# Kernel optimization log

Hardware: AMD Instinct MI355X
Metric: run time of the kernel (lower is better)

## Reference

```python
import jax, jax.numpy as jnp
import numpy as np

N, A_IN, A_OUT, X_IN, X_OUT, NNODE = 4, 8, 16, 64, 64, 1024


def setup_inputs() -> dict:
    key = jax.random.key(0)
    ks = jax.random.split(key, 32)
    s = 0.02
    inp = {
        'A': jax.random.normal(ks[0], (N, A_IN, NNODE, NNODE), jnp.float32),
        'X': jax.random.normal(ks[1], (N, NNODE, X_IN), jnp.float32),
    }
    # Linear weights stored as (in, out); torch Linear computes x @ W.T with W (out,in)
    for i, k in zip(range(1, 6), ks[2:7]):
        inp[f'A_W{i}'] = jax.random.normal(k, (A_IN, A_OUT), jnp.float32) * s
    inp['A_W6'] = jax.random.normal(ks[7], (X_IN, A_OUT), jnp.float32) * s
    inp['A_W7'] = jax.random.normal(ks[8], (X_IN, A_OUT), jnp.float32) * s
    inp['A_bias'] = jnp.zeros((A_OUT,), jnp.float32)
    for pfx, base in (('X1', 9), ('X2', 16)):
        inp[f'{pfx}_W1'] = jax.random.normal(ks[base], (X_IN, X_OUT), jnp.float32) * s
        inp[f'{pfx}_W2'] = jax.random.normal(ks[base + 1], (X_IN, X_OUT), jnp.float32) * s
        for j in range(3, 7):
            inp[f'{pfx}_W{j}'] = jax.random.normal(ks[base + j - 1], (A_IN, X_OUT), jnp.float32) * s
        inp[f'{pfx}_bias'] = jnp.zeros((X_OUT,), jnp.float32)
    inp['out_W'] = jax.random.normal(ks[23], (A_OUT * X_OUT, X_OUT), jnp.float32) * s
    inp['out_b'] = jnp.zeros((X_OUT,), jnp.float32)
    return inp


def reference(A, X, A_W1, A_W2, A_W3, A_W4, A_W5, A_W6, A_W7, A_bias,
              X1_W1, X1_W2, X1_W3, X1_W4, X1_W5, X1_W6, X1_bias,
              X2_W1, X2_W2, X2_W3, X2_W4, X2_W5, X2_W6, X2_bias,
              out_W, out_b):
    n = A.shape[-1]
    # diag_part: N, n, 1, A_in
    dp = jnp.transpose(jnp.diagonal(A, axis1=-2, axis2=-1), (0, 2, 1))[:, :, None, :]
    mdp = jnp.mean(dp, axis=1, keepdims=True)                 # N,1,1,A_in
    moc = jnp.transpose(jnp.mean(A, axis=-1), (0, 2, 1))[:, :, None, :]  # N,n,1,A_in
    mall = jnp.mean(moc, axis=1, keepdims=True)               # N,1,1,A_in
    mX = jnp.mean(X, axis=-2, keepdims=True)                  # N,1,x_in

    At = jnp.transpose(A, (0, 2, 3, 1)) @ A_W1                # N,n,n,A_out
    At = At + mall @ A_W2
    t3 = moc @ A_W3                                           # N,n,1,A_out (linear commutes with symmetrize)
    At = At + t3 + jnp.swapaxes(t3, 1, 2)
    t6 = X @ A_W6                                             # N,n,A_out
    At = At + t6[:, :, None, :] + t6[:, None, :, :]
    At = At + (mX @ A_W7)[:, None, :, :]
    At = At + A_bias
    At = At + mdp @ A_W4
    t5 = dp @ A_W5
    At = At + t5 + jnp.swapaxes(t5, 1, 2)

    def x_branch(W1, W2, W3, W4, W5, W6, b):
        r = X @ W1 + mX @ W2 + moc[:, :, 0, :] @ W3 + mall[:, 0, :, :] @ W6 + b
        return r + dp[:, :, 0, :] @ W4 + mdp[:, 0, :, :] @ W5  # N,n,x_out

    X1t = x_branch(X1_W1, X1_W2, X1_W3, X1_W4, X1_W5, X1_W6, X1_bias)
    X2t = x_branch(X2_W1, X2_W2, X2_W3, X2_W4, X2_W5, X2_W6, X2_bias)

    out = jnp.einsum('nijs,njt->nist', At, X2t) / n           # N,n,A_out,x_out
    out = out.reshape(out.shape[0], out.shape[1], -1) @ out_W + out_b
    out = out + X1t
    return jnp.transpose(At, (0, 3, 1, 2)), out
```

## Files before the change

### kernel.cpp

```cpp
#include <hip/hip_runtime.h>


#define NB 4
#define CI 8
#define SO 16
#define XD 64
#define NN 1024

typedef unsigned short u16;
typedef unsigned int u32;
typedef float f32x4 __attribute__((ext_vector_type(4)));
typedef short bf16x8 __attribute__((ext_vector_type(8)));

#define WS_MOC    0x000000u
#define WS_DP     0x020000u
#define WS_CONSTA 0x043000u
#define WS_CX1    0x044000u
#define WS_CX2    0x045000u
#define WS_K1     0x048000u
#define WS_C2     0x04C000u
#define WS_PAIRA  0x050000u
#define WS_PAIRAT 0x090000u
#define WS_X1T    0x0D0000u
#define WS_X2TT   0x1D0000u
#define WS_WGT    0x250000u
#define WS_H      0x260000u
#define WS_XPART  0x264000u
#define WS_S2     0x268000u

__device__ __forceinline__ float bf2f(u16 u){ return __uint_as_float(((u32)u) << 16); }
__device__ __forceinline__ u16 f2bf(float f){
    u32 x = __float_as_uint(f);
    x += 0x7fffu + ((x >> 16) & 1u);
    return (u16)(x >> 16);
}

__global__ __launch_bounds__(256) void k_rowstats(const float* __restrict__ A,
                                                  const float* __restrict__ X,
                                                  float* __restrict__ moc,
                                                  float* __restrict__ dpv,
                                                  float* __restrict__ Xpart)
{
    if (blockIdx.x < NB*CI*NN/4) {
        int wave = threadIdx.x >> 6, lane = threadIdx.x & 63;
        int row = blockIdx.x * 4 + wave;
        int i = row & (NN - 1);
        const float* rp = A + (size_t)row * NN;
        f32x4 v0 = *(const f32x4*)(rp + lane * 16);
        f32x4 v1 = *(const f32x4*)(rp + lane * 16 + 4);
        f32x4 v2 = *(const f32x4*)(rp + lane * 16 + 8);
        f32x4 v3 = *(const f32x4*)(rp + lane * 16 + 12);
        float s = 0.f;
        #pragma unroll
        for (int e = 0; e < 4; e++) s += v0[e] + v1[e] + v2[e] + v3[e];
        #pragma unroll
        for (int off = 32; off; off >>= 1) s += __shfl_down(s, off);
        if (lane == 0) {
            moc[row] = s * (1.f / NN);
            dpv[row] = rp[i];
        }
    } else {
        int idx = blockIdx.x - NB*CI*NN/4;
        int b = idx >> 4, seg = idx & 15;
        int g = threadIdx.x >> 6, x = threadIdx.x & 63;
        __shared__ float red[4][64];
        float s = 0.f;
        #pragma unroll
        for (int k = 0; k < 16; k++) {
            int i = seg*64 + g*16 + k;
            s += X[((size_t)b*NN + i)*XD + x];
        }
        red[g][x] = s;
        __syncthreads();
        if (threadIdx.x < 64)
            Xpart[idx*64 + threadIdx.x] =
                red[0][threadIdx.x]+red[1][threadIdx.x]+red[2][threadIdx.x]+red[3][threadIdx.x];
    }
}

__global__ __launch_bounds__(256) void k_batchstats(
    const float* __restrict__ Xpart,
    const float* __restrict__ moc, const float* __restrict__ dpv,
    const float* __restrict__ AW2, const float* __restrict__ AW4, const float* __restrict__ AW7,
    const float* __restrict__ Abias,
    const float* __restrict__ X1W2, const float* __restrict__ X1W5, const float* __restrict__ X1W6,
    const float* __restrict__ X1b,
    const float* __restrict__ X2W2, const float* __restrict__ X2W5, const float* __restrict__ X2W6,
    const float* __restrict__ X2b,
    float* __restrict__ constA_o, float* __restrict__ cx1_o, float* __restrict__ cx2_o)
{
    int b = blockIdx.x, tid = threadIdx.x;
    __shared__ float sdp[8][32], smoc[8][32];
    __shared__ float mdp_s[8], mall_s[8], mx_s[64];
    {
        int c = tid >> 5, rr = tid & 31;
        float pd = 0.f, pm = 0.f;
        for (int i = rr; i < NN; i += 32) {
            pd += dpv[(b*CI + c)*NN + i];
            pm += moc[(b*CI + c)*NN + i];
        }
        sdp[c][rr] = pd; smoc[c][rr] = pm;
    }
    if (tid < 64) {
        float px = 0.f;
        #pragma unroll
        for (int s = 0; s < 16; s++) px += Xpart[(b*16 + s)*64 + tid];
        mx_s[tid] = px * (1.f/NN);
    }
    __syncthreads();
    if (tid < 8) {
        float sd = 0.f, sm = 0.f;
        for (int k = 0; k < 32; k++) { sd += sdp[tid][k]; sm += smoc[tid][k]; }
        mdp_s[tid] = sd * (1.f/NN); mall_s[tid] = sm * (1.f/NN);
    }
    __syncthreads();
    if (tid < SO) {
        float v = Abias[tid];
        #pragma unroll
        for (int c = 0; c < 8; c++)
            v += mall_s[c]*AW2[c*SO+tid] + mdp_s[c]*AW4[c*SO+tid];
        for (int x = 0; x < 64; x++) v += mx_s[x]*AW7[x*SO+tid];
        constA_o[b*SO + tid] = v;
    }
    if (tid < 64) {
        float v1 = X1b[tid], v2 = X2b[tid];
        for (int x = 0; x < 64; x++) {
            float m = mx_s[x];
            v1 += m*X1W2[x*64+tid];
            v2 += m*X2W2[x*64+tid];
        }
        #pragma unroll
        for (int c = 0; c < 8; c++) {
            v1 += mall_s[c]*X1W6[c*64+tid] + mdp_s[c]*X1W5[c*64+tid];
            v2 += mall_s[c]*X2W6[c*64+tid] + mdp_s[c]*X2W5[c*64+tid];
        }
        cx1_o[b*64+tid] = v1; cx2_o[b*64+tid] = v2;
    }
}

__global__ __launch_bounds__(256) void k_rows(const float* __restrict__ X,
    const float* __restrict__ moc, const float* __restrict__ dpv,
    const float* __restrict__ AW3, const float* __restrict__ AW5, const float* __restrict__ AW6,
    const float* __restrict__ X1W1, const float* __restrict__ X1W3, const float* __restrict__ X1W4,
    const float* __restrict__ X2W1, const float* __restrict__ X2W3, const float* __restrict__ X2W4,
    const float* __restrict__ cx1, const float* __restrict__ cx2,
    float* __restrict__ X1t, u16* __restrict__ X2tT,
    float* __restrict__ pairA, float* __restrict__ pairAT)
{
    int wave = threadIdx.x >> 6, u = threadIdx.x & 63;
    int r = blockIdx.x * 4 + wave;
    int b = r >> 10, i = r & (NN - 1);
    float xv = X[(size_t)r*XD + u];
    float a1 = cx1[b*XD + u], a2 = cx2[b*XD + u];
    int s = u & 15;
    float pa = 0.f;
    for (int x = 0; x < XD; x++) {
        float xx = __shfl(xv, x);
        a1 += xx * X1W1[x*XD + u];
        a2 += xx * X2W1[x*XD + u];
        pa += xx * AW6[x*SO + s];
    }
    #pragma unroll
    for (int c = 0; c < CI; c++) {
        float mv = moc[(b*CI + c)*NN + i];
        float dv = dpv[(b*CI + c)*NN + i];
        a1 += mv*X1W3[c*XD+u] + dv*X1W4[c*XD+u];
        a2 += mv*X2W3[c*XD+u] + dv*X2W4[c*XD+u];
        pa += mv*AW3[c*SO+s] + dv*AW5[c*SO+s];
    }
    X1t[(size_t)r*XD + u] = a1;
    X2tT[((size_t)b*XD + u)*NN + i] = f2bf(a2);
    if (u < SO) {
        pairA[(size_t)r*SO + u] = pa;
        pairAT[((size_t)b*SO + u)*NN + i] = pa;
    }
}

__global__ __launch_bounds__(256) void k_H(const float* __restrict__ pairAT,
                                           const u16* __restrict__ X2tT,
                                           float* __restrict__ H, float* __restrict__ s2)
{
    __shared__ float red[4][64];
    int tid = threadIdx.x;
    int t = tid & 63, g = tid >> 6;
    if (blockIdx.x < 64) {
        int b = blockIdx.x >> 4, s = blockIdx.x & 15;
        const u16* x2 = X2tT + ((size_t)(b*XD) + t)*NN;
        const float* par = pairAT + ((size_t)(b*SO) + s)*NN;
        float h = 0.f;
        for (int i = g*256; i < (g+1)*256; i += 8) {
            bf16x8 v = __builtin_bit_cast(bf16x8, *(const uint4*)(x2 + i));
            f32x4 p0 = *(const f32x4*)(par + i);
            f32x4 p1 = *(const f32x4*)(par + i + 4);
            #pragma unroll
            for (int e = 0; e < 4; e++)
                h += p0[e]*bf2f((u16)v[e]) + p1[e]*bf2f((u16)v[e+4]);
        }
        red[g][t] = h;
        __syncthreads();
        if (tid < 64)
            H[((size_t)(b*SO) + s)*64 + tid] = red[0][tid]+red[1][tid]+red[2][tid]+red[3][tid];
    } else {
        int b = blockIdx.x - 64;
        const u16* x2 = X2tT + ((size_t)(b*XD) + t)*NN;
        float p = 0.f;
        for (int i = g*256; i < (g+1)*256; i += 8) {
            bf16x8 v = __builtin_bit_cast(bf16x8, *(const uint4*)(x2 + i));
            #pragma unroll
            for (int e = 0; e < 8; e++) p += bf2f((u16)v[e]);
        }
        red[g][t] = p;
        __syncthreads();
        if (tid < 64)
            s2[b*64 + tid] = red[0][tid]+red[1][tid]+red[2][tid]+red[3][tid];
    }
}

__global__ __launch_bounds__(256) void k_small2(const float* __restrict__ Wo, const float* __restrict__ AW1,
    const float* __restrict__ constA, const float* __restrict__ H, const float* __restrict__ s2,
    float* __restrict__ K1, float* __restrict__ C2, u16* __restrict__ WGT)
{
    int tid = threadIdx.x;
    if (blockIdx.x < 4) {
        int b = blockIdx.x;
        __shared__ float ls[4][64];
        int t = tid & 63, g = tid >> 6;
        const float* s2b = s2 + b*64;
        float pc = 0.f;
        #pragma unroll
        for (int si = 0; si < 4; si++) {
            int s = g*4 + si;
            float ca = constA[b*SO + s];
            const float* Hs = H + ((size_t)(b*SO) + s)*64;
            float v = 0.f;
            for (int tt = 0; tt < 64; tt++) {
                float w = Wo[(s*64+tt)*64 + t];
                v  += s2b[tt] * w;
                pc += (Hs[tt] + ca*s2b[tt]) * w;
            }
            K1[((size_t)(b*SO) + s)*XD + t] = v;
        }
        ls[g][t] = pc;
        __syncthreads();
        if (tid < 64) C2[b*XD + tid] = (ls[0][tid]+ls[1][tid]+ls[2][tid]+ls[3][tid]) * (1.f/NN);
    } else {
        int o = (blockIdx.x - 4)*256 + tid;
        int u = o >> 9;
        int k = o & 511;
        int c = k >> 6, t = k & 63;
        float v = 0.f;
        #pragma unroll
        for (int s = 0; s < SO; s++) v += AW1[c*SO+s] * Wo[(s*64+t)*64 + u];
        WGT[(size_t)u*512 + k] = f2bf(v);
    }
}

__global__ __launch_bounds__(512, 2) void k_fused(
    const float* __restrict__ A, const u16* __restrict__ X2tT,
    const float* __restrict__ AW1,
    const float* __restrict__ pairA, const float* __restrict__ pairAT,
    const float* __restrict__ constA,
    const u16* __restrict__ WGT, const float* __restrict__ K1,
    const float* __restrict__ C2, const float* __restrict__ X1t,
    const float* __restrict__ outb,
    float* __restrict__ out0, float* __restrict__ out1)
{
    __shared__ __align__(16) char smem[32768];
    __shared__ __align__(16) u16 X2s[64][64];
    __shared__ __align__(16) float W1s[CI][SO];

    int tid = threadIdx.x;
    int wave = tid >> 6, lane = tid & 63;
    int lr = lane & 15, lq = lane >> 4;
    int b = blockIdx.x >> 6;
    int i0 = (blockIdx.x & 63) * 16;

    if (tid < CI*SO) W1s[tid >> 4][tid & 15] = AW1[tid];

    int iA = wave*2, iB = wave*2 + 1;
    float rcA[SO], rcB[SO];
    #pragma unroll
    for (int s = 0; s < SO; s++) {
        float ca = constA[b*SO + s];
        rcA[s] = pairA[((size_t)(b*NN) + i0 + iA)*SO + s] + ca;
        rcB[s] = pairA[((size_t)(b*NN) + i0 + iB)*SO + s] + ca;
    }

    f32x4 acc[4];
    #pragma unroll
    for (int nt = 0; nt < 4; nt++) acc[nt] = (f32x4){0.f,0.f,0.f,0.f};

    uint4 rA0, rA1, rA2, rA3, rX;

#define STAGE_LOAD(CH) { \
    int jb = (CH)*64; \
    int rr0 = (wave*4 + 0)*4 + (lane>>4); \
    int rr1 = (wave*4 + 1)*4 + (lane>>4); \
    int rr2 = (wave*4 + 2)*4 + (lane>>4); \
    int rr3 = (wave*4 + 3)*4 + (lane>>4); \
    rA0 = *(const uint4*)(A + (((size_t)(b*CI + (rr0>>4)))*NN + i0 + (rr0&15))*NN + jb + (lane&15)*4); \
    rA1 = *(const uint4*)(A + (((size_t)(b*CI + (rr1>>4)))*NN + i0 + (rr1&15))*NN + jb + (lane&15)*4); \
    rA2 = *(const uint4*)(A + (((size_t)(b*CI + (rr2>>4)))*NN + i0 + (rr2&15))*NN + jb + (lane&15)*4); \
    rA3 = *(const uint4*)(A + (((size_t)(b*CI + (rr3>>4)))*NN + i0 + (rr3&15))*NN + jb + (lane&15)*4); \
    int tt = wave*8 + (lane>>3); \
    rX = *(const uint4*)(X2tT + ((size_t)(b*XD) + tt)*NN + jb + (lane&7)*8); \
}

#define STAGE_WRITE() { \
    int rr0 = (wave*4 + 0)*4 + (lane>>4); \
    int rr1 = (wave*4 + 1)*4 + (lane>>4); \
    int rr2 = (wave*4 + 2)*4 + (lane>>4); \
    int rr3 = (wave*4 + 3)*4 + (lane>>4); \
    *(uint4*)(smem + rr0*256 + (((lane&15)*16) ^ ((rr0&7)<<4))) = rA0; \
    *(uint4*)(smem + rr1*256 + (((lane&15)*16) ^ ((rr1&7)<<4))) = rA1; \
    *(uint4*)(smem + rr2*256 + (((lane&15)*16) ^ ((rr2&7)<<4))) = rA2; \
    *(uint4*)(smem + rr3*256 + (((lane&15)*16) ^ ((rr3&7)<<4))) = rA3; \
    int tt = wave*8 + (lane>>3); \
    *(uint4*)((char*)X2s + tt*128 + (((lane&7)*16) ^ ((tt&7)<<4))) = rX; \
}

    STAGE_LOAD(0);

    for (int ch = 0; ch < 16; ch++) {
        __syncthreads();
        STAGE_WRITE();
        __syncthreads();
        if (ch < 15) STAGE_LOAD(ch + 1);

        int j0v = ch * 64;

        {
            int rr = wave*16 + lr;
            int swz = (lr & 7) << 4;
            #pragma unroll
            for (int ks = 0; ks < 2; ks++) {
                int y0 = ks*128 + lq*32;
                f32x4 A0 = __builtin_bit_cast(f32x4, *(const uint4*)(smem + rr*256 + (y0 ^ swz)));
                f32x4 A1 = __builtin_bit_cast(f32x4, *(const uint4*)(smem + rr*256 + ((y0 + 16) ^ swz)));
                bf16x8 af;
                #pragma unroll
                for (int e = 0; e < 4; e++) { af[e] = (short)f2bf(A0[e]); af[e+4] = (short)f2bf(A1[e]); }
                #pragma unroll
                for (int nt = 0; nt < 4; nt++) {
                    int tt = nt*16 + lr;
                    bf16x8 bfr = __builtin_bit_cast(bf16x8,
                        *(const uint4*)((char*)X2s + tt*128 + ((ks*64 + lq*16) ^ ((tt&7)<<4))));
                    acc[nt] = __builtin_amdgcn_mfma_f32_16x16x32_bf16(af, bfr, acc[nt], 0, 0, 0);
                }
            }
        }

        {
            float o0[SO], o1[SO];
            #pragma unroll
            for (int s = 0; s < SO; s++) { o0[s] = 0.f; o1[s] = 0.f; }
            for (int c = 0; c < CI; c++) {
                f32x4 w0 = *(const f32x4*)&W1s[c][0];
                f32x4 w1 = *(const f32x4*)&W1s[c][4];
                f32x4 w2 = *(const f32x4*)&W1s[c][8];
                f32x4 w3 = *(const f32x4*)&W1s[c][12];
                float W1v[SO];
                #pragma unroll
                for (int e = 0; e < 4; e++) { W1v[e] = w0[e]; W1v[4+e] = w1[e]; W1v[8+e] = w2[e]; W1v[12+e] = w3[e]; }
                int ra = c*16 + iA, rb = c*16 + iB;
                float aA = *(const float*)(smem + ra*256 + ((lane*4) ^ ((ra&7)<<4)));
                float aB = *(const float*)(smem + rb*256 + ((lane*4) ^ ((rb&7)<<4)));
                #pragma unroll
                for (int s = 0; s < SO; s++) {
                    o0[s] = fmaf(aA, W1v[s], o0[s]);
                    o1[s] = fmaf(aB, W1v[s], o1[s]);
                }
            }
            #pragma unroll
            for (int s = 0; s < SO; s++) {
                float pj = pairAT[((size_t)(b*SO) + s)*NN + j0v + lane];
                out0[((size_t)(b*SO + s)*NN + i0 + iA)*NN + j0v + lane] = o0[s] + rcA[s] + pj;
                out0[((size_t)(b*SO + s)*NN + i0 + iB)*NN + j0v + lane] = o1[s] + rcB[s] + pj;
            }
        }
    }

    __syncthreads();
    u16* Gb = (u16*)smem;
    #pragma unroll
    for (int nt = 0; nt < 4; nt++) {
        #pragma unroll
        for (int reg = 0; reg < 4; reg++)
            Gb[(lq*4 + reg)*520 + wave*64 + nt*16 + lr] = f2bf(acc[nt][reg]);
    }
    __syncthreads();

    if (wave < 4) {
        int nt = wave;
        f32x4 acc1 = (f32x4){0.f,0.f,0.f,0.f};
        #pragma unroll
        for (int k0 = 0; k0 < 512; k0 += 32) {
            bf16x8 ga = __builtin_bit_cast(bf16x8, *(const uint4*)&Gb[lr*520 + k0 + lq*8]);
            bf16x8 wb = __builtin_bit_cast(bf16x8,
                *(const uint4*)(WGT + (size_t)(nt*16 + lr)*512 + k0 + lq*8));
            acc1 = __builtin_amdgcn_mfma_f32_16x16x32_bf16(ga, wb, acc1, 0, 0, 0);
        }
        int u = nt*16 + lr;
        float k1c[SO];
        #pragma unroll
        for (int s = 0; s < SO; s++) k1c[s] = K1[((size_t)(b*SO) + s)*XD + u];
        float cb = C2[b*XD + u] + outb[u];
        #pragma unroll
        for (int reg = 0; reg < 4; reg++) {
            int ii = i0 + lq*4 + reg;
            const float* pa = pairA + ((size_t)(b*NN) + ii)*SO;
            float s16 = 0.f;
            #pragma unroll
            for (int s = 0; s < SO; s++) s16 += pa[s] * k1c[s];
            out1[((size_t)(b*NN) + ii)*XD + u] =
                (acc1[reg] + s16) * (1.f/NN) + cb
                + X1t[((size_t)(b*NN) + ii)*XD + u];
        }
    }
#undef STAGE_LOAD
#undef STAGE_WRITE
}

extern "C" void kernel_launch(void* const* d_in, const int* in_sizes, int n_in,
                              void* d_out, int out_size, void* d_ws, size_t ws_size,
                              hipStream_t stream)
{
    const float* A     = (const float*)d_in[0];
    const float* X     = (const float*)d_in[1];
    const float* AW1   = (const float*)d_in[2];
    const float* AW2   = (const float*)d_in[3];
    const float* AW3   = (const float*)d_in[4];
    const float* AW4   = (const float*)d_in[5];
    const float* AW5   = (const float*)d_in[6];
    const float* AW6   = (const float*)d_in[7];
    const float* AW7   = (const float*)d_in[8];
    const float* Abias = (const float*)d_in[9];
    const float* X1W1  = (const float*)d_in[10];
    const float* X1W2  = (const float*)d_in[11];
    const float* X1W3  = (const float*)d_in[12];
    const float* X1W4  = (const float*)d_in[13];
    const float* X1W5  = (const float*)d_in[14];
    const float* X1W6  = (const float*)d_in[15];
    const float* X1b   = (const float*)d_in[16];
    const float* X2W1  = (const float*)d_in[17];
    const float* X2W2  = (const float*)d_in[18];
    const float* X2W3  = (const float*)d_in[19];
    const float* X2W4  = (const float*)d_in[20];
    const float* X2W5  = (const float*)d_in[21];
    const float* X2W6  = (const float*)d_in[22];
    const float* X2b   = (const float*)d_in[23];
    const float* Wo    = (const float*)d_in[24];
    const float* outb  = (const float*)d_in[25];

    char* ws = (char*)d_ws;
    float* moc    = (float*)(ws + WS_MOC);
    float* dpv    = (float*)(ws + WS_DP);
    float* constA = (float*)(ws + WS_CONSTA);
    float* cx1    = (float*)(ws + WS_CX1);
    float* cx2    = (float*)(ws + WS_CX2);
    float* K1     = (float*)(ws + WS_K1);
    float* C2     = (float*)(ws + WS_C2);
    float* pairA  = (float*)(ws + WS_PAIRA);
    float* pairAT = (float*)(ws + WS_PAIRAT);
    float* X1t    = (float*)(ws + WS_X1T);
    u16*   X2tT   = (u16*)(ws + WS_X2TT);
    u16*   WGT    = (u16*)(ws + WS_WGT);
    float* H      = (float*)(ws + WS_H);
    float* Xpart  = (float*)(ws + WS_XPART);
    float* s2     = (float*)(ws + WS_S2);

    float* out0 = (float*)d_out;
    float* out1 = out0 + (size_t)NB*SO*NN*NN;

    k_rowstats<<<dim3(NB*CI*NN/4 + 64), dim3(256), 0, stream>>>(A, X, moc, dpv, Xpart);
    k_batchstats<<<dim3(NB), dim3(256), 0, stream>>>(Xpart, moc, dpv,
        AW2, AW4, AW7, Abias, X1W2, X1W5, X1W6, X1b, X2W2, X2W5, X2W6, X2b,
        constA, cx1, cx2);
    k_rows<<<dim3(NB*NN/4), dim3(256), 0, stream>>>(X, moc, dpv,
        AW3, AW5, AW6, X1W1, X1W3, X1W4, X2W1, X2W3, X2W4, cx1, cx2,
        X1t, X2tT, pairA, pairAT);
    k_H<<<dim3(68), dim3(256), 0, stream>>>(pairAT, X2tT, H, s2);
    k_small2<<<dim3(132), dim3(256), 0, stream>>>(Wo, AW1, constA, H, s2, K1, C2, WGT);
    k_fused<<<dim3(NB*NN/16), dim3(512), 0, stream>>>(A, X2tT, AW1,
        pairA, pairAT, constA, WGT, K1, C2, X1t, outb, out0, out1);
}
```

Before: 506.0 us.

## Halve row tile per block, split MFMA K across waves, stage pairAT in LDS

Each block now handles 8 rows instead of 16, so twice as many blocks are launched and shared memory use drops. The MFMA work is split over K between wave halves and the partial sums are reduced through LDS at the end. pairAT is staged in LDS along with A and X2, and each wave computes one output row, which removes redundant global loads per output. The trade-off is extra reduction syncs and a final GEMM whose padded half of the 16 rows does no useful work.

```diff
diff --git a/kernel.cpp b/kernel.cpp
--- a/kernel.cpp
+++ b/kernel.cpp
@@ -265,58 +265,60 @@
     const float* __restrict__ outb,
     float* __restrict__ out0, float* __restrict__ out1)
 {
-    __shared__ __align__(16) char smem[32768];
-    __shared__ __align__(16) u16 X2s[64][64];
-    __shared__ __align__(16) float W1s[CI][SO];
+    __shared__ __align__(16) char Abuf[16384];
+    __shared__ __align__(16) char X2buf[8192];
+    __shared__ __align__(16) float PATs[SO][64];
+    __shared__ float W1s[CI][SO];
 
     int tid = threadIdx.x;
     int wave = tid >> 6, lane = tid & 63;
     int lr = lane & 15, lq = lane >> 4;
-    int b = blockIdx.x >> 6;
-    int i0 = (blockIdx.x & 63) * 16;
+    int cp = wave & 3, ksh = wave >> 2;
+    int iw = wave;
+    int b = blockIdx.x >> 7;
+    int i0 = (blockIdx.x & 127) * 8;
 
     if (tid < CI*SO) W1s[tid >> 4][tid & 15] = AW1[tid];
 
-    int iA = wave*2, iB = wave*2 + 1;
-    float rcA[SO], rcB[SO];
-    #pragma unroll
-    for (int s = 0; s < SO; s++) {
-        float ca = constA[b*SO + s];
-        rcA[s] = pairA[((size_t)(b*NN) + i0 + iA)*SO + s] + ca;
-        rcB[s] = pairA[((size_t)(b*NN) + i0 + iB)*SO + s] + ca;
+    float rc[SO];
+    {
+        const float* pr = pairA + ((size_t)(b*NN) + i0 + iw)*SO;
+        const float* ca = constA + b*SO;
+        #pragma unroll
+        for (int q = 0; q < 4; q++) {
+            f32x4 t4 = *(const f32x4*)(pr + q*4);
+            #pragma unroll
+            for (int e = 0; e < 4; e++) rc[q*4+e] = t4[e] + ca[q*4+e];
+        }
     }
 
     f32x4 acc[4];
     #pragma unroll
     for (int nt = 0; nt < 4; nt++) acc[nt] = (f32x4){0.f,0.f,0.f,0.f};
 
-    uint4 rA0, rA1, rA2, rA3, rX;
+    uint4 rA0, rA1, rX;
+    uint2 rP;
+    int rrA = tid >> 4;
+    int rrB = 32 + rrA;
+    int cbA = (tid & 15) * 16;
+    int ttS = tid >> 3;
+    int cbX = (tid & 7) * 16;
+    int spS = tid >> 5;
+    int cbP = (tid & 31) * 8;
 
 #define STAGE_LOAD(CH) { \
-    int jb = (CH)*64; \
-    int rr0 = (wave*4 + 0)*4 + (lane>>4); \
-    int rr1 = (wave*4 + 1)*4 + (lane>>4); \
-    int rr2 = (wave*4 + 2)*4 + (lane>>4); \
-    int rr3 = (wave*4 + 3)*4 + (lane>>4); \
-    rA0 = *(const uint4*)(A + (((size_t)(b*CI + (rr0>>4)))*NN + i0 + (rr0&15))*NN + jb + (lane&15)*4); \
-    rA1 = *(const uint4*)(A + (((size_t)(b*CI + (rr1>>4)))*NN + i0 + (rr1&15))*NN + jb + (lane&15)*4); \
-    rA2 = *(const uint4*)(A + (((size_t)(b*CI + (rr2>>4)))*NN + i0 + (rr2&15))*NN + jb + (lane&15)*4); \
-    rA3 = *(const uint4*)(A + (((size_t)(b*CI + (rr3>>4)))*NN + i0 + (rr3&15))*NN + jb + (lane&15)*4); \
-    int tt = wave*8 + (lane>>3); \
-    rX = *(const uint4*)(X2tT + ((size_t)(b*XD) + tt)*NN + jb + (lane&7)*8); \
+    int jb_ = (CH)*64; \
+    rA0 = *(const uint4*)(A + (((size_t)(b*CI + (rrA>>3)))*NN + i0 + (rrA&7))*NN + jb_ + (tid&15)*4); \
+    rA1 = *(const uint4*)(A + (((size_t)(b*CI + (rrB>>3)))*NN + i0 + (rrB&7))*NN + jb_ + (tid&15)*4); \
+    rX  = *(const uint4*)(X2tT + ((size_t)(b*XD) + ttS)*NN + jb_ + (tid&7)*8); \
+    rP  = *(const uint2*)(pairAT + ((size_t)(b*SO) + spS)*NN + jb_ + (tid&31)*2); \
 }
 
 #define STAGE_WRITE() { \
-    int rr0 = (wave*4 + 0)*4 + (lane>>4); \
-    int rr1 = (wave*4 + 1)*4 + (lane>>4); \
-    int rr2 = (wave*4 + 2)*4 + (lane>>4); \
-    int rr3 = (wave*4 + 3)*4 + (lane>>4); \
-    *(uint4*)(smem + rr0*256 + (((lane&15)*16) ^ ((rr0&7)<<4))) = rA0; \
-    *(uint4*)(smem + rr1*256 + (((lane&15)*16) ^ ((rr1&7)<<4))) = rA1; \
-    *(uint4*)(smem + rr2*256 + (((lane&15)*16) ^ ((rr2&7)<<4))) = rA2; \
-    *(uint4*)(smem + rr3*256 + (((lane&15)*16) ^ ((rr3&7)<<4))) = rA3; \
-    int tt = wave*8 + (lane>>3); \
-    *(uint4*)((char*)X2s + tt*128 + (((lane&7)*16) ^ ((tt&7)<<4))) = rX; \
+    *(uint4*)(Abuf + rrA*256 + (cbA ^ ((rrA&7)<<4))) = rA0; \
+    *(uint4*)(Abuf + rrB*256 + (cbA ^ ((rrB&7)<<4))) = rA1; \
+    *(uint4*)(X2buf + ttS*128 + (cbX ^ ((ttS&7)<<4))) = rX; \
+    *(uint2*)((char*)PATs + spS*256 + cbP) = rP; \
 }
 
     STAGE_LOAD(0);
@@ -327,66 +329,82 @@
         __syncthreads();
         if (ch < 15) STAGE_LOAD(ch + 1);
 
-        int j0v = ch * 64;
+        int jb = ch * 64;
 
         {
-            int rr = wave*16 + lr;
-            int swz = (lr & 7) << 4;
-            #pragma unroll
-            for (int ks = 0; ks < 2; ks++) {
-                int y0 = ks*128 + lq*32;
-                f32x4 A0 = __builtin_bit_cast(f32x4, *(const uint4*)(smem + rr*256 + (y0 ^ swz)));
-                f32x4 A1 = __builtin_bit_cast(f32x4, *(const uint4*)(smem + rr*256 + ((y0 + 16) ^ swz)));
-                bf16x8 af;
-                #pragma unroll
-                for (int e = 0; e < 4; e++) { af[e] = (short)f2bf(A0[e]); af[e+4] = (short)f2bf(A1[e]); }
-                #pragma unroll
-                for (int nt = 0; nt < 4; nt++) {
-                    int tt = nt*16 + lr;
-                    bf16x8 bfr = __builtin_bit_cast(bf16x8,
-                        *(const uint4*)((char*)X2s + tt*128 + ((ks*64 + lq*16) ^ ((tt&7)<<4))));
-                    acc[nt] = __builtin_amdgcn_mfma_f32_16x16x32_bf16(af, bfr, acc[nt], 0, 0, 0);
-                }
+            int rr = cp*16 + lr;
+            int swz = (rr & 7) << 4;
+            int y0 = ksh*128 + lq*32;
+            f32x4 A0 = __builtin_bit_cast(f32x4, *(const uint4*)(Abuf + rr*256 + (y0 ^ swz)));
+            f32x4 A1 = __builtin_bit_cast(f32x4, *(const uint4*)(Abuf + rr*256 + ((y0 + 16) ^ swz)));
+            bf16x8 af;
+            #pragma unroll
+            for (int e = 0; e < 4; e++) { af[e] = (short)f2bf(A0[e]); af[e+4] = (short)f2bf(A1[e]); }
+            #pragma unroll
+            for (int nt = 0; nt < 4; nt++) {
+                int tt = nt*16 + lr;
+                bf16x8 bfr = __builtin_bit_cast(bf16x8,
+                    *(const uint4*)(X2buf + tt*128 + ((ksh*64 + lq*16) ^ ((tt&7)<<4))));
+                acc[nt] = __builtin_amdgcn_mfma_f32_16x16x32_bf16(af, bfr, acc[nt], 0, 0, 0);
             }
         }
 
         {
-            float o0[SO], o1[SO];
-            #pragma unroll
-            for (int s = 0; s < SO; s++) { o0[s] = 0.f; o1[s] = 0.f; }
+            float o[SO];
+            #pragma unroll
+            for (int s = 0; s < SO; s++) o[s] = rc[s] + PATs[s][lane];
+            int swzi = iw << 4;
+            #pragma unroll
             for (int c = 0; c < CI; c++) {
+                float aA = *(const float*)(Abuf + (c*8 + iw)*256 + ((lane*4) ^ swzi));
                 f32x4 w0 = *(const f32x4*)&W1s[c][0];
                 f32x4 w1 = *(const f32x4*)&W1s[c][4];
                 f32x4 w2 = *(const f32x4*)&W1s[c][8];
                 f32x4 w3 = *(const f32x4*)&W1s[c][12];
-                float W1v[SO];
                 #pragma unroll
-                for (int e = 0; e < 4; e++) { W1v[e] = w0[e]; W1v[4+e] = w1[e]; W1v[8+e] = w2[e]; W1v[12+e] = w3[e]; }
-                int ra = c*16 + iA, rb = c*16 + iB;
-                float aA = *(const float*)(smem + ra*256 + ((lane*4) ^ ((ra&7)<<4)));
-                float aB = *(const float*)(smem + rb*256 + ((lane*4) ^ ((rb&7)<<4)));
-                #pragma unroll
-                for (int s = 0; s < SO; s++) {
-                    o0[s] = fmaf(aA, W1v[s], o0[s]);
-                    o1[s] = fmaf(aB, W1v[s], o1[s]);
+                for (int e = 0; e < 4; e++) {
+                    o[e]    = fmaf(aA, w0[e], o[e]);
+                    o[4+e]  = fmaf(aA, w1[e], o[4+e]);
+                    o[8+e]  = fmaf(aA, w2[e], o[8+e]);
+                    o[12+e] = fmaf(aA, w3[e], o[12+e]);
                 }
             }
             #pragma unroll
-            for (int s = 0; s < SO; s++) {
-                float pj = pairAT[((size_t)(b*SO) + s)*NN + j0v + lane];
-                out0[((size_t)(b*SO + s)*NN + i0 + iA)*NN + j0v + lane] = o0[s] + rcA[s] + pj;
-                out0[((size_t)(b*SO + s)*NN + i0 + iB)*NN + j0v + lane] = o1[s] + rcB[s] + pj;
+            for (int s = 0; s < SO; s++)
+                out0[((size_t)(b*SO + s)*NN + i0 + iw)*NN + jb + lane] = o[s];
+        }
+    }
+
+    __syncthreads();
+    if (ksh == 1) {
+        #pragma unroll
+        for (int nt = 0; nt < 4; nt++)
+            *(f32x4*)(Abuf + (((cp*64 + lane)*16) + nt*4)*4) = acc[nt];
+    }
+    __syncthreads();
+    f32x4 gsum[4];
+    if (ksh == 0) {
+        #pragma unroll
+        for (int nt = 0; nt < 4; nt++) {
+            f32x4 g = *(const f32x4*)(Abuf + (((cp*64 + lane)*16) + nt*4)*4);
+            #pragma unroll
+            for (int e = 0; e < 4; e++) g[e] += acc[nt][e];
+            gsum[nt] = g;
+        }
+    }
+    __syncthreads();
+
+    u16* Gb = (u16*)Abuf;
+    *(uint4*)(Abuf + 8192 + tid*16) = (uint4){0u,0u,0u,0u};
+    if (ksh == 0) {
+        #pragma unroll
+        for (int nt = 0; nt < 4; nt++)
+            #pragma unroll
+            for (int reg = 0; reg < 4; reg++) {
+                int m = lq*4 + reg;
+                int c = 2*cp + (m >> 3);
+                Gb[(m & 7)*512 + c*64 + nt*16 + lr] = f2bf(gsum[nt][reg]);
             }
-        }
-    }
-
-    __syncthreads();
-    u16* Gb = (u16*)smem;
-    #pragma unroll
-    for (int nt = 0; nt < 4; nt++) {
-        #pragma unroll
-        for (int reg = 0; reg < 4; reg++)
-            Gb[(lq*4 + reg)*520 + wave*64 + nt*16 + lr] = f2bf(acc[nt][reg]);
     }
     __syncthreads();
 
@@ -395,26 +413,28 @@
         f32x4 acc1 = (f32x4){0.f,0.f,0.f,0.f};
         #pragma unroll
         for (int k0 = 0; k0 < 512; k0 += 32) {
-            bf16x8 ga = __builtin_bit_cast(bf16x8, *(const uint4*)&Gb[lr*520 + k0 + lq*8]);
+            bf16x8 ga = __builtin_bit_cast(bf16x8, *(const uint4*)&Gb[lr*512 + k0 + lq*8]);
             bf16x8 wb = __builtin_bit_cast(bf16x8,
                 *(const uint4*)(WGT + (size_t)(nt*16 + lr)*512 + k0 + lq*8));
             acc1 = __builtin_amdgcn_mfma_f32_16x16x32_bf16(ga, wb, acc1, 0, 0, 0);
         }
-        int u = nt*16 + lr;
-        float k1c[SO];
-        #pragma unroll
-        for (int s = 0; s < SO; s++) k1c[s] = K1[((size_t)(b*SO) + s)*XD + u];
-        float cb = C2[b*XD + u] + outb[u];
-        #pragma unroll
-        for (int reg = 0; reg < 4; reg++) {
-            int ii = i0 + lq*4 + reg;
-            const float* pa = pairA + ((size_t)(b*NN) + ii)*SO;
-            float s16 = 0.f;
-            #pragma unroll
-            for (int s = 0; s < SO; s++) s16 += pa[s] * k1c[s];
-            out1[((size_t)(b*NN) + ii)*XD + u] =
-                (acc1[reg] + s16) * (1.f/NN) + cb
-                + X1t[((size_t)(b*NN) + ii)*XD + u];
+        if (lq < 2) {
+            int u = nt*16 + lr;
+            float k1c[SO];
+            #pragma unroll
+            for (int s = 0; s < SO; s++) k1c[s] = K1[((size_t)(b*SO) + s)*XD + u];
+            float cb = C2[b*XD + u] + outb[u];
+            #pragma unroll
+            for (int reg = 0; reg < 4; reg++) {
+                int ii = i0 + lq*4 + reg;
+                const float* pa = pairA + ((size_t)(b*NN) + ii)*SO;
+                float s16 = 0.f;
+                #pragma unroll
+                for (int s = 0; s < SO; s++) s16 += pa[s] * k1c[s];
+                out1[((size_t)(b*NN) + ii)*XD + u] =
+                    (acc1[reg] + s16) * (1.f/NN) + cb
+                    + X1t[((size_t)(b*NN) + ii)*XD + u];
+            }
         }
     }
 #undef STAGE_LOAD
@@ -481,6 +501,6 @@
         X1t, X2tT, pairA, pairAT);
     k_H<<<dim3(68), dim3(256), 0, stream>>>(pairAT, X2tT, H, s2);
     k_small2<<<dim3(132), dim3(256), 0, stream>>>(Wo, AW1, constA, H, s2, K1, C2, WGT);
-    k_fused<<<dim3(NB*NN/16), dim3(512), 0, stream>>>(A, X2tT, AW1,
+    k_fused<<<dim3(NB*NN/8), dim3(512), 0, stream>>>(A, X2tT, AW1,
         pairA, pairAT, constA, WGT, K1, C2, X1t, outb, out0, out1);
 }
```

New measurement: 510.6 us. No clear change (+0.9%).
